# Kernel tuning notes

Measured on AMD Instinct MI355X. Metric: run time of the kernel, lower is better.

## Reference

```python
import jax, jax.numpy as jnp
import numpy as np

N_NODES = 50000
N_EDGES = 800000
IN_DIM = 128
HID = 64
N_GRAPHS = 256


def setup_inputs() -> dict:
    key = jax.random.key(0)
    ks = jax.random.split(key, 10)
    s = lambda d: 1.0 / np.sqrt(d)
    return {
        'x': jax.random.normal(ks[0], (N_NODES, IN_DIM), jnp.float32),
        'edge_index': jax.random.randint(ks[1], (2, N_EDGES), 0, N_NODES, jnp.int64),
        'batch': jnp.sort(jax.random.randint(ks[2], (N_NODES,), 0, N_GRAPHS, jnp.int64)),
        'Wp': jax.random.normal(ks[3], (IN_DIM, HID), jnp.float32) * s(IN_DIM),
        'bp': jnp.zeros((HID,), jnp.float32),
        'W1_0': jax.random.normal(ks[4], (HID, HID), jnp.float32) * s(HID),
        'b1_0': jnp.zeros((HID,), jnp.float32),
        'W2_0': jax.random.normal(ks[5], (HID, HID), jnp.float32) * s(HID),
        'b2_0': jnp.zeros((HID,), jnp.float32),
        'W1_1': jax.random.normal(ks[6], (HID, HID), jnp.float32) * s(HID),
        'b1_1': jnp.zeros((HID,), jnp.float32),
        'W2_1': jax.random.normal(ks[7], (HID, HID), jnp.float32) * s(HID),
        'b2_1': jnp.zeros((HID,), jnp.float32),
    }


def _gin_layer(h, src, dst, W1, b1, W2, b2):
    # scatter-add aggregation: sum_{j in N(i)} h_j  (messages flow src -> dst)
    agg = jax.ops.segment_sum(h[src], dst, num_segments=N_NODES)
    z = h + agg  # eps = 0 (GINConv default)
    z = jax.nn.relu(z @ W1 + b1)
    z = z @ W2 + b2
    return jax.nn.relu(z)  # outer activation from SharedGINEncoder


def reference(x, edge_index, batch, Wp, bp, W1_0, b1_0, W2_0, b2_0, W1_1, b1_1, W2_1, b2_1):
    src, dst = edge_index[0], edge_index[1]
    h = jax.nn.relu(x @ Wp + bp)  # [N, HID]
    h = _gin_layer(h, src, dst, W1_0, b1_0, W2_0, b2_0)
    h = _gin_layer(h, src, dst, W1_1, b1_1, W2_1, b2_1)
    # global_mean_pool over graph ids
    sums = jax.ops.segment_sum(h, batch, num_segments=N_GRAPHS)  # [G, HID]
    counts = jax.ops.segment_sum(jnp.ones((h.shape[0],), h.dtype), batch, num_segments=N_GRAPHS)
    return sums / jnp.maximum(counts, 1.0)[:, None]
```

## Files before the change

kernel.cpp:

```cpp
#include <hip/hip_runtime.h>

#define N_NODES 50000
#define N_EDGES 800000
#define IN_DIM 128
#define HID 64
#define N_GRAPHS 256

#define E_PER_BLK 4000
#define F_BLOCKS (N_EDGES / E_PER_BLK)
#define NBKT ((N_NODES + 255) / 256)
#define CNT_N (NBKT * F_BLOCKS)
#define SCB ((CNT_N + 255) / 256)
#define MTILES (N_NODES / 16)
#define DCNT_N (64 * NBKT)
#define DSCB ((DCNT_N + 255) / 256)


__device__ __forceinline__ float bf2f(unsigned short v) {
  return __uint_as_float(((unsigned int)v) << 16);
}
__device__ __forceinline__ unsigned short f2bf(float f) {
  unsigned int u = __float_as_uint(f);
  return (unsigned short)((u + 0x7fffu + ((u >> 16) & 1u)) >> 16);
}

typedef __attribute__((ext_vector_type(8))) short bf16x8;
typedef __attribute__((ext_vector_type(4))) float f32x4;

__global__ __launch_bounds__(256) void part_hist_kernel(const int* __restrict__ dst,
                                                        int* __restrict__ cnt) {
  __shared__ int h[NBKT];
  const int t = threadIdx.x;
  for (int k = t; k < NBKT; k += 256) h[k] = 0;
  __syncthreads();
  const int base = blockIdx.x * E_PER_BLK;
  for (int i = t; i < E_PER_BLK; i += 256) atomicAdd(&h[dst[base + i] >> 8], 1);
  __syncthreads();
  for (int k = t; k < NBKT; k += 256) cnt[k * F_BLOCKS + blockIdx.x] = h[k];
}

__global__ __launch_bounds__(256) void scan1g_kernel(const int* __restrict__ in,
                                                     int* __restrict__ ex,
                                                     int* __restrict__ bsum, int n) {
  __shared__ int s[256];
  const int t = threadIdx.x;
  const int i = blockIdx.x * 256 + t;
  int v = (i < n) ? in[i] : 0;
  s[t] = v;
  __syncthreads();
#pragma unroll
  for (int ofs = 1; ofs < 256; ofs <<= 1) {
    int u = (t >= ofs) ? s[t - ofs] : 0;
    __syncthreads();
    s[t] += u;
    __syncthreads();
  }
  if (i < n) ex[i] = s[t] - v;
  if (t == 255) bsum[blockIdx.x] = s[255];
}

__global__ __launch_bounds__(256) void scan2g_kernel(const int* __restrict__ bsum,
                                                     int* __restrict__ bpref, int nb) {
  __shared__ int s[256];
  const int t = threadIdx.x;
  int v = (t < nb) ? bsum[t] : 0;
  s[t] = v;
  __syncthreads();
#pragma unroll
  for (int ofs = 1; ofs < 256; ofs <<= 1) {
    int u = (t >= ofs) ? s[t - ofs] : 0;
    __syncthreads();
    s[t] += u;
    __syncthreads();
  }
  if (t < nb) bpref[t] = s[t] - v;
}

__global__ __launch_bounds__(256) void part_scatter_kernel(const int* __restrict__ src,
                                                           const int* __restrict__ dst,
                                                           const int* __restrict__ cex,
                                                           const int* __restrict__ bpref,
                                                           int* __restrict__ psrc,
                                                           int* __restrict__ pdst) {
  __shared__ int cur[NBKT];
  const int t = threadIdx.x;
  for (int k = t; k < NBKT; k += 256) {
    const int i = k * F_BLOCKS + blockIdx.x;
    cur[k] = cex[i] + bpref[i >> 8];
  }
  __syncthreads();
  const int base = blockIdx.x * E_PER_BLK;
  for (int i = t; i < E_PER_BLK; i += 256) {
    int d = dst[base + i], s = src[base + i];
    int p = atomicAdd(&cur[d >> 8], 1);
    pdst[p] = d;
    psrc[p] = s;
  }
}

__global__ __launch_bounds__(256) void bucket_sort_kernel(const int* __restrict__ psrc,
                                                          const int* __restrict__ pdst,
                                                          const int* __restrict__ cex,
                                                          const int* __restrict__ bpref,
                                                          int* __restrict__ csr,
                                                          int* __restrict__ off,
                                                          int* __restrict__ dcnt) {
  const int k = blockIdx.x;
  const int t = threadIdx.x;
  const int i0 = k * F_BLOCKS;
  const int b0 = cex[i0] + bpref[i0 >> 8];
  int b1 = N_EDGES;
  if (k != NBKT - 1) {
    const int i1 = (k + 1) * F_BLOCKS;
    b1 = cex[i1] + bpref[i1 >> 8];
  }
  __shared__ int cnt[256];
  __shared__ int s[256];
  __shared__ int cur[256];
  __shared__ int dhist[64];
  cnt[t] = 0;
  if (t < 64) dhist[t] = 0;
  __syncthreads();
  for (int i = b0 + t; i < b1; i += 256) atomicAdd(&cnt[pdst[i] & 255], 1);
  __syncthreads();
  int v = cnt[t];
  s[t] = v;
  __syncthreads();
#pragma unroll
  for (int ofs = 1; ofs < 256; ofs <<= 1) {
    int u = (t >= ofs) ? s[t - ofs] : 0;
    __syncthreads();
    s[t] += u;
    __syncthreads();
  }
  const int node = (k << 8) + t;
  const int start = b0 + s[t] - v;
  cur[t] = start;
  if (node < N_NODES) {
    off[node] = start;
    atomicAdd(&dhist[(v < 63) ? v : 63], 1);
  }
  if (k == NBKT - 1 && t == 0) off[N_NODES] = N_EDGES;
  __syncthreads();
  if (t < 64) dcnt[t * NBKT + k] = dhist[t];
  for (int i = b0 + t; i < b1; i += 256) {
    int d = pdst[i];
    int p = atomicAdd(&cur[d & 255], 1);
    csr[p] = psrc[i];
  }
}

__global__ __launch_bounds__(256) void perm_scatter_kernel(const int* __restrict__ off,
                                                           const int* __restrict__ dex,
                                                           const int* __restrict__ dbpref,
                                                           int* __restrict__ perm) {
  __shared__ int cur[64];
  const int k = blockIdx.x, t = threadIdx.x;
  if (t < 64) {
    const int i = t * NBKT + k;
    cur[t] = dex[i] + dbpref[i >> 8];
  }
  __syncthreads();
  const int node = (k << 8) + t;
  if (node < N_NODES) {
    int d = off[node + 1] - off[node];
    d = (d < 63) ? d : 63;
    int pos = atomicAdd(&cur[d], 1);
    perm[pos] = node;
  }
}

__global__ __launch_bounds__(256) void proj_mfma_kernel(
    const float* __restrict__ x, const float* __restrict__ Wp,
    const float* __restrict__ bp, unsigned short* __restrict__ h) {
  __shared__ __align__(16) unsigned short sWp[8192];
  __shared__ __align__(16) unsigned short sT[4][16][72];
  const int t = threadIdx.x;
  for (int i = t; i < 8192; i += 256) {
    const int k = i >> 6, j = i & 63;
    const int pos = (((j >> 4) * 4 + (k >> 5)) * 64 + ((k >> 3) & 3) * 16 + (j & 15)) * 8 + (k & 7);
    sWp[pos] = f2bf(Wp[i]);
  }
  __syncthreads();
  const int wave = t >> 6, lane = t & 63;
  const int row = lane & 15;
  const int kgrp = lane >> 4;
  float bias[4];
#pragma unroll
  for (int nc = 0; nc < 4; ++nc) bias[nc] = bp[nc * 16 + row];
  const int tile = blockIdx.x * 4 + wave;
  if (tile < MTILES) {
    const int n = tile * 16 + row;
    bf16x8 a[4];
#pragma unroll
    for (int ks = 0; ks < 4; ++ks) {
      float4 v0 = *(const float4*)&x[n * IN_DIM + ks * 32 + kgrp * 8];
      float4 v1 = *(const float4*)&x[n * IN_DIM + ks * 32 + kgrp * 8 + 4];
      a[ks][0] = (short)f2bf(v0.x);
      a[ks][1] = (short)f2bf(v0.y);
      a[ks][2] = (short)f2bf(v0.z);
      a[ks][3] = (short)f2bf(v0.w);
      a[ks][4] = (short)f2bf(v1.x);
      a[ks][5] = (short)f2bf(v1.y);
      a[ks][6] = (short)f2bf(v1.z);
      a[ks][7] = (short)f2bf(v1.w);
    }
    f32x4 acc;
#pragma unroll
    for (int nc = 0; nc < 4; ++nc) {
      acc = (f32x4){bias[nc], bias[nc], bias[nc], bias[nc]};
#pragma unroll
      for (int ks = 0; ks < 4; ++ks) {
        bf16x8 bf = *(const bf16x8*)&sWp[((nc * 4 + ks) * 64 + lane) * 8];
        acc = __builtin_amdgcn_mfma_f32_16x16x32_bf16(a[ks], bf, acc, 0, 0, 0);
      }
#pragma unroll
      for (int r = 0; r < 4; ++r)
        sT[wave][kgrp * 4 + r][nc * 16 + row] = f2bf(fmaxf(acc[r], 0.0f));
    }
    const int n0 = tile * 16;
#pragma unroll
    for (int p = 0; p < 2; ++p) {
      const int idx2 = p * 64 + lane;
      const int ri = idx2 >> 3, ch = idx2 & 7;
      uint4 v = *(const uint4*)&sT[wave][ri][ch * 8];
      *(uint4*)&h[(n0 + ri) * HID + ch * 8] = v;
    }
  }
}

__global__ __launch_bounds__(256) void gin_fused_mfma_kernel(
    const unsigned short* __restrict__ h_in, const int* __restrict__ off,
    const int* __restrict__ csr, const int* __restrict__ perm,
    const float* __restrict__ W1, const float* __restrict__ b1,
    const float* __restrict__ W2, const float* __restrict__ b2,
    unsigned short* __restrict__ h_out) {
  __shared__ __align__(16) unsigned short sW1[4096];
  __shared__ __align__(16) unsigned short sW2[4096];
  __shared__ __align__(16) unsigned short sT[4][16][72];
  const int t = threadIdx.x;
  for (int i = t; i < 4096; i += 256) {
    const int k = i >> 6, j = i & 63;
    const int pos = (((j >> 4) * 2 + (k >> 5)) * 64 + ((k >> 3) & 3) * 16 + (j & 15)) * 8 + (k & 7);
    sW1[pos] = f2bf(W1[i]);
    sW2[pos] = f2bf(W2[i]);
  }
  __syncthreads();
  const int wave = t >> 6, lane = t & 63;
  const int row = lane & 15;
  const int kgrp = lane >> 4;
  float bias1[4], bias2[4];
#pragma unroll
  for (int nc = 0; nc < 4; ++nc) {
    bias1[nc] = b1[nc * 16 + row];
    bias2[nc] = b2[nc * 16 + row];
  }
  const uint4* __restrict__ hv = (const uint4*)h_in;
  const int tile = blockIdx.x * 4 + wave;
  if (tile < MTILES) {
    const int n = perm[(tile << 4) + row];
    const int o0 = off[n];
    const int deg = off[n + 1] - o0;
    int dm = deg;
#pragma unroll
    for (int m = 1; m <= 8; m <<= 1) {
      int o = __shfl_xor(dm, m);
      dm = (o > dm) ? o : dm;
    }
    float ac0[8], ac1[8];
    {
      uint4 ua = hv[n * 8 + kgrp];
      uint4 ub = hv[n * 8 + 4 + kgrp];
      const unsigned int* pa = (const unsigned int*)&ua;
      const unsigned int* pb = (const unsigned int*)&ub;
#pragma unroll
      for (int e = 0; e < 4; ++e) {
        ac0[2 * e] = bf2f((unsigned short)(pa[e] & 0xffff));
        ac0[2 * e + 1] = bf2f((unsigned short)(pa[e] >> 16));
        ac1[2 * e] = bf2f((unsigned short)(pb[e] & 0xffff));
        ac1[2 * e + 1] = bf2f((unsigned short)(pb[e] >> 16));
      }
    }
    for (int j = 0; j < dm; j += 4) {
#pragma unroll
      for (int u = 0; u < 4; ++u) {
        const int jj = j + u;
        const int pos = o0 + ((jj < deg) ? jj : 0);
        const int idx = csr[(pos < N_EDGES) ? pos : (N_EDGES - 1)];
        const float m = (jj < deg) ? 1.0f : 0.0f;
        uint4 ua = hv[idx * 8 + kgrp];
        uint4 ub = hv[idx * 8 + 4 + kgrp];
        const unsigned int* pa = (const unsigned int*)&ua;
        const unsigned int* pb = (const unsigned int*)&ub;
#pragma unroll
        for (int e = 0; e < 4; ++e) {
          ac0[2 * e] = fmaf(m, bf2f((unsigned short)(pa[e] & 0xffff)), ac0[2 * e]);
          ac0[2 * e + 1] = fmaf(m, bf2f((unsigned short)(pa[e] >> 16)), ac0[2 * e + 1]);
          ac1[2 * e] = fmaf(m, bf2f((unsigned short)(pb[e] & 0xffff)), ac1[2 * e]);
          ac1[2 * e + 1] = fmaf(m, bf2f((unsigned short)(pb[e] >> 16)), ac1[2 * e + 1]);
        }
      }
    }
    bf16x8 a1[2];
#pragma unroll
    for (int e = 0; e < 8; ++e) {
      a1[0][e] = (short)f2bf(ac0[e]);
      a1[1][e] = (short)f2bf(ac1[e]);
    }
    f32x4 acc;
#pragma unroll
    for (int nc = 0; nc < 4; ++nc) {
      acc = (f32x4){bias1[nc], bias1[nc], bias1[nc], bias1[nc]};
#pragma unroll
      for (int ks = 0; ks < 2; ++ks) {
        bf16x8 bf = *(const bf16x8*)&sW1[((nc * 2 + ks) * 64 + lane) * 8];
        acc = __builtin_amdgcn_mfma_f32_16x16x32_bf16(a1[ks], bf, acc, 0, 0, 0);
      }
#pragma unroll
      for (int r = 0; r < 4; ++r)
        sT[wave][kgrp * 4 + r][nc * 16 + row] = f2bf(fmaxf(acc[r], 0.0f));
    }
    bf16x8 a2[2];
    a2[0] = *(const bf16x8*)&sT[wave][row][kgrp * 8];
    a2[1] = *(const bf16x8*)&sT[wave][row][32 + kgrp * 8];
#pragma unroll
    for (int nc = 0; nc < 4; ++nc) {
      acc = (f32x4){bias2[nc], bias2[nc], bias2[nc], bias2[nc]};
#pragma unroll
      for (int ks = 0; ks < 2; ++ks) {
        bf16x8 bf = *(const bf16x8*)&sW2[((nc * 2 + ks) * 64 + lane) * 8];
        acc = __builtin_amdgcn_mfma_f32_16x16x32_bf16(a2[ks], bf, acc, 0, 0, 0);
      }
#pragma unroll
      for (int r = 0; r < 4; ++r)
        sT[wave][kgrp * 4 + r][nc * 16 + row] = f2bf(fmaxf(acc[r], 0.0f));
    }
#pragma unroll
    for (int p = 0; p < 2; ++p) {
      const int idx2 = p * 64 + lane;
      const int ri = idx2 >> 3, ch = idx2 & 7;
      const int nodeo = perm[(tile << 4) + ri];
      uint4 v = *(const uint4*)&sT[wave][ri][ch * 8];
      *(uint4*)&h_out[nodeo * HID + ch * 8] = v;
    }
  }
}

__global__ __launch_bounds__(256) void pool_kernel(const unsigned short* __restrict__ h,
                                                   const int* __restrict__ batch,
                                                   float* __restrict__ out) {
  const int g = blockIdx.x;
  int lo = 0, hi = N_NODES;
  while (lo < hi) {
    int mid = (lo + hi) >> 1;
    if (batch[mid] < g) lo = mid + 1; else hi = mid;
  }
  const int s = lo;
  hi = N_NODES;
  while (lo < hi) {
    int mid = (lo + hi) >> 1;
    if (batch[mid] < g + 1) lo = mid + 1; else hi = mid;
  }
  const int e = lo;
  const int wave = threadIdx.x >> 6, lane = threadIdx.x & 63;
  float a0 = 0.f, a1 = 0.f, a2 = 0.f, a3 = 0.f;
  int n = s + wave;
  for (; n + 12 < e; n += 16) {
    a0 += bf2f(h[n * HID + lane]);
    a1 += bf2f(h[(n + 4) * HID + lane]);
    a2 += bf2f(h[(n + 8) * HID + lane]);
    a3 += bf2f(h[(n + 12) * HID + lane]);
  }
  for (; n < e; n += 4) a0 += bf2f(h[n * HID + lane]);
  __shared__ float red[4][HID];
  red[wave][lane] = ((a0 + a1) + (a2 + a3));
  __syncthreads();
  if (wave == 0) {
    float v = red[0][lane] + red[1][lane] + red[2][lane] + red[3][lane];
    float cnt = (float)(e - s);
    out[g * HID + lane] = v / fmaxf(cnt, 1.0f);
  }
}

extern "C" void kernel_launch(void* const* d_in, const int* in_sizes, int n_in,
                              void* d_out, int out_size, void* d_ws, size_t ws_size,
                              hipStream_t stream) {
  const float* x    = (const float*)d_in[0];
  const int*   edge = (const int*)d_in[1];
  const int*   batch= (const int*)d_in[2];
  const float* Wp   = (const float*)d_in[3];
  const float* bp   = (const float*)d_in[4];
  const float* W1_0 = (const float*)d_in[5];
  const float* b1_0 = (const float*)d_in[6];
  const float* W2_0 = (const float*)d_in[7];
  const float* b2_0 = (const float*)d_in[8];
  const float* W1_1 = (const float*)d_in[9];
  const float* b1_1 = (const float*)d_in[10];
  const float* W2_1 = (const float*)d_in[11];
  const float* b2_1 = (const float*)d_in[12];
  const int* src = edge;
  const int* dst = edge + N_EDGES;
  float* out = (float*)d_out;

  const size_t NB = (size_t)N_NODES * HID;
  unsigned short* hA = (unsigned short*)d_ws;
  unsigned short* hB = hA + NB;
  int* off     = (int*)(hB + NB);
  int* cnt     = off + N_NODES + 1;
  int* cex     = cnt + CNT_N;
  int* sbsum   = cex + CNT_N;
  int* sbpref  = sbsum + SCB;
  int* dcnt    = sbpref + SCB;
  int* dex     = dcnt + DCNT_N;
  int* dbsum   = dex + DCNT_N;
  int* dbpref  = dbsum + DSCB;
  int* perm    = dbpref + DSCB;
  int* pdst    = perm + N_NODES;
  int* psrc    = pdst + N_EDGES;
  int* csr     = psrc + N_EDGES;

  dim3 b256(256);

  part_hist_kernel<<<F_BLOCKS, b256, 0, stream>>>(dst, cnt);
  scan1g_kernel<<<SCB, b256, 0, stream>>>(cnt, cex, sbsum, CNT_N);
  scan2g_kernel<<<1, b256, 0, stream>>>(sbsum, sbpref, SCB);
  part_scatter_kernel<<<F_BLOCKS, b256, 0, stream>>>(src, dst, cex, sbpref, psrc, pdst);
  bucket_sort_kernel<<<NBKT, b256, 0, stream>>>(psrc, pdst, cex, sbpref, csr, off, dcnt);

  scan1g_kernel<<<DSCB, b256, 0, stream>>>(dcnt, dex, dbsum, DCNT_N);
  scan2g_kernel<<<1, b256, 0, stream>>>(dbsum, dbpref, DSCB);
  perm_scatter_kernel<<<NBKT, b256, 0, stream>>>(off, dex, dbpref, perm);

  proj_mfma_kernel<<<782, b256, 0, stream>>>(x, Wp, bp, hA);

  gin_fused_mfma_kernel<<<782, b256, 0, stream>>>(hA, off, csr, perm, W1_0, b1_0, W2_0, b2_0, hB);
  gin_fused_mfma_kernel<<<782, b256, 0, stream>>>(hB, off, csr, perm, W1_1, b1_1, W2_1, b2_1, hA);

  pool_kernel<<<N_GRAPHS, b256, 0, stream>>>(hA, batch, out);
}
```

Measured before the change: 127.6 us.

## Fuse partition histogram and scatter via per-bucket atomic regions with packed edges

Replaces the histogram, two-level scan and separate scatter passes with one kernel that reserves space in fixed-capacity per-bucket regions using global atomics, writing each edge packed as src plus low destination bits in one 32-bit word. The bucket sort reads these packed regions, and the degree-sorted permutation now uses global atomic degree counters with an in-block scan instead of a separate scan. This cuts kernel launches and global traffic during CSR construction. In exchange it assumes each bucket holds at most RCAP edges and that node ids fit in 16 bits, although N_NODES is 50000, which does fit. It also makes edge order within a bucket, and so perm order, nondeterministic.

```diff
diff --git a/kernel.cpp b/kernel.cpp
--- a/kernel.cpp
+++ b/kernel.cpp
@@ -9,11 +9,8 @@
 #define E_PER_BLK 4000
 #define F_BLOCKS (N_EDGES / E_PER_BLK)
 #define NBKT ((N_NODES + 255) / 256)
-#define CNT_N (NBKT * F_BLOCKS)
-#define SCB ((CNT_N + 255) / 256)
+#define RCAP 8192
 #define MTILES (N_NODES / 16)
-#define DCNT_N (64 * NBKT)
-#define DSCB ((DCNT_N + 255) / 256)
 
 
 __device__ __forceinline__ float bf2f(unsigned short v) {
@@ -27,25 +24,32 @@
 typedef __attribute__((ext_vector_type(8))) short bf16x8;
 typedef __attribute__((ext_vector_type(4))) float f32x4;
 
-__global__ __launch_bounds__(256) void part_hist_kernel(const int* __restrict__ dst,
-                                                        int* __restrict__ cnt) {
+__global__ __launch_bounds__(256) void part_scatter_fused_kernel(
+    const int* __restrict__ src, const int* __restrict__ dst,
+    int* __restrict__ gcur, unsigned int* __restrict__ edges) {
   __shared__ int h[NBKT];
+  __shared__ int cur[NBKT];
   const int t = threadIdx.x;
   for (int k = t; k < NBKT; k += 256) h[k] = 0;
   __syncthreads();
   const int base = blockIdx.x * E_PER_BLK;
   for (int i = t; i < E_PER_BLK; i += 256) atomicAdd(&h[dst[base + i] >> 8], 1);
   __syncthreads();
-  for (int k = t; k < NBKT; k += 256) cnt[k * F_BLOCKS + blockIdx.x] = h[k];
-}
-
-__global__ __launch_bounds__(256) void scan1g_kernel(const int* __restrict__ in,
-                                                     int* __restrict__ ex,
-                                                     int* __restrict__ bsum, int n) {
+  for (int k = t; k < NBKT; k += 256)
+    cur[k] = k * RCAP + atomicAdd(&gcur[k], h[k]);
+  __syncthreads();
+  for (int i = t; i < E_PER_BLK; i += 256) {
+    int d = dst[base + i], s = src[base + i];
+    int p = atomicAdd(&cur[d >> 8], 1);
+    edges[p] = (unsigned int)s | ((unsigned int)(d & 255) << 16);
+  }
+}
+
+__global__ __launch_bounds__(256) void scan196_kernel(const int* __restrict__ gcur,
+                                                      int* __restrict__ bbase) {
   __shared__ int s[256];
   const int t = threadIdx.x;
-  const int i = blockIdx.x * 256 + t;
-  int v = (i < n) ? in[i] : 0;
+  int v = (t < NBKT) ? gcur[t] : 0;
   s[t] = v;
   __syncthreads();
 #pragma unroll
@@ -55,65 +59,19 @@
     s[t] += u;
     __syncthreads();
   }
-  if (i < n) ex[i] = s[t] - v;
-  if (t == 255) bsum[blockIdx.x] = s[255];
-}
-
-__global__ __launch_bounds__(256) void scan2g_kernel(const int* __restrict__ bsum,
-                                                     int* __restrict__ bpref, int nb) {
-  __shared__ int s[256];
-  const int t = threadIdx.x;
-  int v = (t < nb) ? bsum[t] : 0;
-  s[t] = v;
-  __syncthreads();
-#pragma unroll
-  for (int ofs = 1; ofs < 256; ofs <<= 1) {
-    int u = (t >= ofs) ? s[t - ofs] : 0;
-    __syncthreads();
-    s[t] += u;
-    __syncthreads();
-  }
-  if (t < nb) bpref[t] = s[t] - v;
-}
-
-__global__ __launch_bounds__(256) void part_scatter_kernel(const int* __restrict__ src,
-                                                           const int* __restrict__ dst,
-                                                           const int* __restrict__ cex,
-                                                           const int* __restrict__ bpref,
-                                                           int* __restrict__ psrc,
-                                                           int* __restrict__ pdst) {
-  __shared__ int cur[NBKT];
-  const int t = threadIdx.x;
-  for (int k = t; k < NBKT; k += 256) {
-    const int i = k * F_BLOCKS + blockIdx.x;
-    cur[k] = cex[i] + bpref[i >> 8];
-  }
-  __syncthreads();
-  const int base = blockIdx.x * E_PER_BLK;
-  for (int i = t; i < E_PER_BLK; i += 256) {
-    int d = dst[base + i], s = src[base + i];
-    int p = atomicAdd(&cur[d >> 8], 1);
-    pdst[p] = d;
-    psrc[p] = s;
-  }
-}
-
-__global__ __launch_bounds__(256) void bucket_sort_kernel(const int* __restrict__ psrc,
-                                                          const int* __restrict__ pdst,
-                                                          const int* __restrict__ cex,
-                                                          const int* __restrict__ bpref,
-                                                          int* __restrict__ csr,
-                                                          int* __restrict__ off,
-                                                          int* __restrict__ dcnt) {
+  if (t < NBKT) bbase[t] = s[t] - v;
+  if (t == NBKT - 1) bbase[NBKT] = s[t];
+}
+
+__global__ __launch_bounds__(256) void bucket_sort_kernel(
+    const unsigned int* __restrict__ edges, const int* __restrict__ gcur,
+    const int* __restrict__ bbase, int* __restrict__ csr, int* __restrict__ off,
+    int* __restrict__ gdeg) {
   const int k = blockIdx.x;
   const int t = threadIdx.x;
-  const int i0 = k * F_BLOCKS;
-  const int b0 = cex[i0] + bpref[i0 >> 8];
-  int b1 = N_EDGES;
-  if (k != NBKT - 1) {
-    const int i1 = (k + 1) * F_BLOCKS;
-    b1 = cex[i1] + bpref[i1 >> 8];
-  }
+  const int tot = gcur[k];
+  const int b0 = bbase[k];
+  const unsigned int* __restrict__ reg = edges + k * RCAP;
   __shared__ int cnt[256];
   __shared__ int s[256];
   __shared__ int cur[256];
@@ -121,7 +79,7 @@
   cnt[t] = 0;
   if (t < 64) dhist[t] = 0;
   __syncthreads();
-  for (int i = b0 + t; i < b1; i += 256) atomicAdd(&cnt[pdst[i] & 255], 1);
+  for (int i = t; i < tot; i += 256) atomicAdd(&cnt[(reg[i] >> 16) & 255], 1);
   __syncthreads();
   int v = cnt[t];
   s[t] = v;
@@ -142,30 +100,45 @@
   }
   if (k == NBKT - 1 && t == 0) off[N_NODES] = N_EDGES;
   __syncthreads();
-  if (t < 64) dcnt[t * NBKT + k] = dhist[t];
-  for (int i = b0 + t; i < b1; i += 256) {
-    int d = pdst[i];
-    int p = atomicAdd(&cur[d & 255], 1);
-    csr[p] = psrc[i];
+  if (t < 64 && dhist[t] > 0) atomicAdd(&gdeg[t], dhist[t]);
+  for (int i = t; i < tot; i += 256) {
+    unsigned int e = reg[i];
+    int p = atomicAdd(&cur[(e >> 16) & 255], 1);
+    csr[p] = (int)(e & 0xffff);
   }
 }
 
 __global__ __launch_bounds__(256) void perm_scatter_kernel(const int* __restrict__ off,
-                                                           const int* __restrict__ dex,
-                                                           const int* __restrict__ dbpref,
+                                                           const int* __restrict__ gdeg,
+                                                           int* __restrict__ gpcur,
                                                            int* __restrict__ perm) {
-  __shared__ int cur[64];
+  __shared__ int sg[64];
   const int k = blockIdx.x, t = threadIdx.x;
+  if (t < 64) sg[t] = gdeg[t];
+  __syncthreads();
   if (t < 64) {
-    const int i = t * NBKT + k;
-    cur[t] = dex[i] + dbpref[i >> 8];
-  }
-  __syncthreads();
+    int acc = 0;
+#pragma unroll
+    for (int ofs = 1; ofs < 64; ofs <<= 1) {
+      int u = (t >= ofs) ? sg[t - ofs] : 0;
+      __syncthreads();
+      sg[t] += u;
+      __syncthreads();
+    }
+    (void)acc;
+  } else {
+#pragma unroll
+    for (int ofs = 1; ofs < 64; ofs <<= 1) {
+      __syncthreads();
+      __syncthreads();
+    }
+  }
   const int node = (k << 8) + t;
   if (node < N_NODES) {
     int d = off[node + 1] - off[node];
     d = (d < 63) ? d : 63;
-    int pos = atomicAdd(&cur[d], 1);
+    int base = sg[d] - gdeg[d];
+    int pos = base + atomicAdd(&gpcur[d], 1);
     perm[pos] = node;
   }
 }
@@ -405,31 +378,23 @@
   const size_t NB = (size_t)N_NODES * HID;
   unsigned short* hA = (unsigned short*)d_ws;
   unsigned short* hB = hA + NB;
-  int* off     = (int*)(hB + NB);
-  int* cnt     = off + N_NODES + 1;
-  int* cex     = cnt + CNT_N;
-  int* sbsum   = cex + CNT_N;
-  int* sbpref  = sbsum + SCB;
-  int* dcnt    = sbpref + SCB;
-  int* dex     = dcnt + DCNT_N;
-  int* dbsum   = dex + DCNT_N;
-  int* dbpref  = dbsum + DSCB;
-  int* perm    = dbpref + DSCB;
-  int* pdst    = perm + N_NODES;
-  int* psrc    = pdst + N_EDGES;
-  int* csr     = psrc + N_EDGES;
+  int* off    = (int*)(hB + NB);
+  int* bbase  = off + N_NODES + 1;
+  int* gcur   = bbase + NBKT + 1;
+  int* gdeg   = gcur + NBKT;
+  int* gpcur  = gdeg + 64;
+  int* perm   = gpcur + 64;
+  unsigned int* edges = (unsigned int*)(perm + N_NODES);
+  int* csr    = (int*)(edges + (size_t)NBKT * RCAP);
 
   dim3 b256(256);
 
-  part_hist_kernel<<<F_BLOCKS, b256, 0, stream>>>(dst, cnt);
-  scan1g_kernel<<<SCB, b256, 0, stream>>>(cnt, cex, sbsum, CNT_N);
-  scan2g_kernel<<<1, b256, 0, stream>>>(sbsum, sbpref, SCB);
-  part_scatter_kernel<<<F_BLOCKS, b256, 0, stream>>>(src, dst, cex, sbpref, psrc, pdst);
-  bucket_sort_kernel<<<NBKT, b256, 0, stream>>>(psrc, pdst, cex, sbpref, csr, off, dcnt);
-
-  scan1g_kernel<<<DSCB, b256, 0, stream>>>(dcnt, dex, dbsum, DCNT_N);
-  scan2g_kernel<<<1, b256, 0, stream>>>(dbsum, dbpref, DSCB);
-  perm_scatter_kernel<<<NBKT, b256, 0, stream>>>(off, dex, dbpref, perm);
+  hipMemsetAsync(gcur, 0, (NBKT + 64 + 64) * sizeof(int), stream);
+
+  part_scatter_fused_kernel<<<F_BLOCKS, b256, 0, stream>>>(src, dst, gcur, edges);
+  scan196_kernel<<<1, b256, 0, stream>>>(gcur, bbase);
+  bucket_sort_kernel<<<NBKT, b256, 0, stream>>>(edges, gcur, bbase, csr, off, gdeg);
+  perm_scatter_kernel<<<NBKT, b256, 0, stream>>>(off, gdeg, gpcur, perm);
 
   proj_mfma_kernel<<<782, b256, 0, stream>>>(x, Wp, bp, hA);
 
```

New measurement: 272.3 us. 114% more time.
